# Kernel tuning notes

Hardware: AMD Instinct MI355X
Metric: run time of the kernel (lower is better)

## Reference

```python
import jax, jax.numpy as jnp
import numpy as np

DIM = 256
N_EMBED = 8192
DECAY = 0.1
COMMITMENT = 1.0
EPS = 1e-05


def setup_inputs() -> dict:
    key = jax.random.key(0)
    k1, k2, k3, k4 = jax.random.split(key, 4)
    return {
        "input": jax.random.normal(k1, (8, 1024, DIM), dtype=jnp.float32),
        "embed": jax.random.normal(k2, (DIM, N_EMBED), dtype=jnp.float32),
        "cluster_size": jax.random.uniform(k3, (N_EMBED,), dtype=jnp.float32),
        "embed_avg": jax.random.normal(k4, (DIM, N_EMBED), dtype=jnp.float32),
    }


def reference(input, embed, cluster_size, embed_avg):
    dtype = input.dtype
    flatten = input.reshape(-1, DIM)  # [N, dim]
    # squared euclidean distance to each code: [N, n_embed]
    dist = (
        jnp.sum(flatten * flatten, axis=1, keepdims=True)
        - 2.0 * (flatten @ embed)
        + jnp.sum(embed * embed, axis=0, keepdims=True)
    )
    embed_ind_flat = jnp.argmin(dist, axis=1)  # [N]
    embed_ind = embed_ind_flat.reshape(input.shape[:-1])
    quantize = jnp.take(embed.T, embed_ind, axis=0)  # [..., dim]

    # EMA codebook update (training path), via segment sums instead of dense one-hot
    bins = jax.ops.segment_sum(
        jnp.ones_like(embed_ind_flat, dtype=dtype), embed_ind_flat, num_segments=N_EMBED
    )  # one_hot.sum(0)
    embed_sum = jax.ops.segment_sum(flatten, embed_ind_flat, num_segments=N_EMBED).T  # [dim, n_embed]
    cluster_size_new = cluster_size * DECAY + (1.0 - DECAY) * bins
    embed_avg_new = embed_avg * DECAY + (1.0 - DECAY) * embed_sum
    smoothed = (cluster_size_new + EPS) / (jnp.sum(cluster_size_new) + N_EMBED * EPS)
    cs = smoothed * jnp.sum(cluster_size_new)
    embed_normalized = embed_avg_new / cs[None, :]

    commit_loss = jnp.mean((jax.lax.stop_gradient(quantize) - input) ** 2) * COMMITMENT
    quantize_st = input + jax.lax.stop_gradient(quantize - input)
    return (quantize_st, embed_ind, commit_loss, embed_normalized, cluster_size_new, embed_avg_new)
```

## Files before the change

### kernel.cpp

```cpp
#include <hip/hip_runtime.h>

typedef unsigned short u16;
typedef __attribute__((ext_vector_type(8))) short short8;
typedef __attribute__((ext_vector_type(4))) float f32x4;

#define DIM    256
#define NE     8192
#define NROWS  8192
#define DECAY  0.1f
#define EPS_F  1e-5f
#define CRANGES 16
#define CPH     8
#define MQ      384u

#define OUT_Q    0
#define OUT_IND  2097152
#define OUT_LOSS 2105344
#define OUT_NORM 2105345
#define OUT_CSN  4202497
#define OUT_AVG  4210689

#define WS_CAND  65536
#define WS_ENORM 1114112
#define WS_BASEQ 1146880
#define WS_SUM   1179648
#define WS_BINS  9568256
#define WS_LOSS  9601024
#define WS_SCS   9601032
#define WS_XB    9601040
#define WS_ETB   13795344
#define WS_ET32  17989648
#define WS_ZLEN  (WS_XB - WS_SUM)

__device__ __forceinline__ unsigned f32_ord(float f)
{
    unsigned u = __float_as_uint(f);
    return (u & 0x80000000u) ? ~u : (u | 0x80000000u);
}
__device__ __forceinline__ u16 bf16rne(float f)
{
    unsigned u = __float_as_uint(f);
    return (u16)((u + 0x7fffu + ((u >> 16) & 1u)) >> 16);
}
__device__ __forceinline__ void gload16(const void* g, void* l)
{
    __builtin_amdgcn_global_load_lds((const __attribute__((address_space(1))) unsigned int*)g,
                                     (__attribute__((address_space(3))) unsigned int*)l, 16, 0, 0);
}

__global__ __launch_bounds__(256) void vq_prep_k(const float* __restrict__ X,
                                                 const float* __restrict__ E,
                                                 const float* __restrict__ CS,
                                                 u16* __restrict__ Xb,
                                                 float* __restrict__ ET32,
                                                 u16* __restrict__ ETb,
                                                 float* __restrict__ enorm,
                                                 float* __restrict__ baseq,
                                                 double* __restrict__ sumcs)
{
    const int bid = blockIdx.x;
    const int t = threadIdx.x;

    if (bid < 128) {
        __shared__ float T[64][65];
        const int j0 = bid * 64;
        const int jc = t >> 2, seg = t & 3;
        const int j = j0 + jc;
        float esum = 0.f;
        for (int d0 = 0; d0 < DIM; d0 += 64) {
            if (d0) __syncthreads();
            #pragma unroll
            for (int p = 0; p < 4; ++p) {
                const int dr = p * 16 + (t >> 4);
                const float4 v = *(const float4*)(E + (size_t)(d0 + dr) * NE + j0 + (t & 15) * 4);
                T[dr][(t & 15) * 4 + 0] = v.x; T[dr][(t & 15) * 4 + 1] = v.y;
                T[dr][(t & 15) * 4 + 2] = v.z; T[dr][(t & 15) * 4 + 3] = v.w;
            }
            __syncthreads();
            float vals[16];
            #pragma unroll
            for (int i = 0; i < 16; ++i) vals[i] = T[seg * 16 + i][jc];
            float4* o32 = (float4*)(ET32 + (size_t)j * DIM + d0 + seg * 16);
            o32[0] = make_float4(vals[0], vals[1], vals[2], vals[3]);
            o32[1] = make_float4(vals[4], vals[5], vals[6], vals[7]);
            o32[2] = make_float4(vals[8], vals[9], vals[10], vals[11]);
            o32[3] = make_float4(vals[12], vals[13], vals[14], vals[15]);
            short8 b0, b1;
            #pragma unroll
            for (int i = 0; i < 8; ++i) { b0[i] = (short)bf16rne(vals[i]); b1[i] = (short)bf16rne(vals[8 + i]); }
            *(short8*)(ETb + (size_t)j * DIM + d0 + seg * 16) = b0;
            *(short8*)(ETb + (size_t)j * DIM + d0 + seg * 16 + 8) = b1;
            #pragma unroll
            for (int i = 0; i < 16; ++i) esum += vals[i] * vals[i];
        }
        esum += __shfl_xor(esum, 1, 4);
        esum += __shfl_xor(esum, 2, 4);
        if (seg == 0) {
            enorm[j] = esum;
            baseq[j] = (esum + 512.f) * 256.f;
        }
    } else if (bid < 256) {
        const int chunk = bid - 128;
        #pragma unroll
        for (int it = 0; it < 8; ++it) {
            const int gi = chunk * 2048 + it * 256 + t;
            const float4 a = ((const float4*)X)[gi * 2];
            const float4 b = ((const float4*)X)[gi * 2 + 1];
            short8 v;
            v[0] = (short)bf16rne(a.x); v[1] = (short)bf16rne(a.y);
            v[2] = (short)bf16rne(a.z); v[3] = (short)bf16rne(a.w);
            v[4] = (short)bf16rne(b.x); v[5] = (short)bf16rne(b.y);
            v[6] = (short)bf16rne(b.z); v[7] = (short)bf16rne(b.w);
            *(short8*)(Xb + (size_t)gi * 8) = v;
        }
    } else {
        double s = 0.0;
        #pragma unroll
        for (int it = 0; it < 8; ++it) {
            const float4 v = ((const float4*)CS)[it * 256 + t];
            s += (double)v.x + (double)v.y + (double)v.z + (double)v.w;
        }
        #pragma unroll
        for (int off = 32; off > 0; off >>= 1) s += __shfl_down(s, off);
        __shared__ double wred[4];
        if ((t & 63) == 0) wred[t >> 6] = s;
        __syncthreads();
        if (t == 0) sumcs[0] = wred[0] + wred[1] + wred[2] + wred[3];
    }
}

__global__ __launch_bounds__(256, 2) void vq_scan_k(const u16* __restrict__ Xb,
                                                    const u16* __restrict__ ETb,
                                                    const float* __restrict__ baseq,
                                                    unsigned* __restrict__ cand)
{
    __shared__ u16 Bs[2][32][512];

    const int tid = threadIdx.x;
    const int w = tid >> 6, l = tid & 63;
    const int lane16 = l & 15, g = l >> 4;
    const int rowbase = blockIdx.x * 256 + w * 64;
    const int c0 = blockIdx.y * 512;

    short8 af[4][8];
    #pragma unroll
    for (int sub = 0; sub < 4; ++sub)
        #pragma unroll
        for (int k8 = 0; k8 < 8; ++k8) {
            af[sub][k8] = *(const short8*)(Xb + (size_t)(rowbase + sub * 16 + lane16) * DIM + k8 * 32 + g * 8);
            asm volatile("" : "+a"(af[sub][k8]));
        }

    unsigned s0[16], s1[16];
    #pragma unroll
    for (int i = 0; i < 16; ++i) { s0[i] = 0xFFFFFFFFu; s1[i] = 0xFFFFFFFFu; }

    const u16* gsrc = ETb + (size_t)(c0 + lane16) * DIM + (size_t)w * 64 + g * 8;

    #pragma unroll
    for (int tt = 0; tt < 4; ++tt) {
        gload16(gsrc + (size_t)tt * 16 * DIM,      &Bs[0][tt * 8 + 2 * w + 0][0]);
        gload16(gsrc + (size_t)tt * 16 * DIM + 32, &Bs[0][tt * 8 + 2 * w + 1][0]);
    }
    asm volatile("s_waitcnt vmcnt(0)" ::: "memory");
    __builtin_amdgcn_s_barrier();

    int buf = 0;
    #pragma unroll 1
    for (int p = 0; p < CPH; ++p) {
        if (p + 1 < CPH) {
            const u16* nsrc = gsrc + (size_t)(p + 1) * 64 * DIM;
            #pragma unroll
            for (int tt = 0; tt < 4; ++tt) {
                gload16(nsrc + (size_t)tt * 16 * DIM,      &Bs[buf ^ 1][tt * 8 + 2 * w + 0][0]);
                gload16(nsrc + (size_t)tt * 16 * DIM + 32, &Bs[buf ^ 1][tt * 8 + 2 * w + 1][0]);
            }
        }
        #pragma unroll
        for (int half = 0; half < 4; ++half) {
            const int col = c0 + (p * 4 + half) * 16 + lane16;
            const float bq = baseq[col];
            f32x4 acc[4];
            #pragma unroll
            for (int sub = 0; sub < 4; ++sub) acc[sub] = {0.f, 0.f, 0.f, 0.f};
            __builtin_amdgcn_s_setprio(1);
            #pragma unroll
            for (int k8 = 0; k8 < 8; ++k8) {
                const short8 bf = *(const short8*)&Bs[buf][half * 8 + k8][l * 8];
                #pragma unroll
                for (int sub = 0; sub < 4; ++sub)
                    acc[sub] = __builtin_amdgcn_mfma_f32_16x16x32_bf16(af[sub][k8], bf, acc[sub], 0, 0, 0);
            }
            __builtin_amdgcn_s_setprio(0);
            #pragma unroll
            for (int sub = 0; sub < 4; ++sub)
                #pragma unroll
                for (int r = 0; r < 4; ++r) {
                    const int i = sub * 4 + r;
                    const float qf = fmaf(acc[sub][r], -512.f, bq);
                    const unsigned key = (((unsigned)qf) << 13) | (unsigned)col;
                    const unsigned tt = max(s0[i], key);
                    s0[i] = min(s0[i], key);
                    s1[i] = min(s1[i], tt);
                }
        }
        asm volatile("s_waitcnt vmcnt(0)" ::: "memory");
        __builtin_amdgcn_s_barrier();
        buf ^= 1;
    }

    #pragma unroll
    for (int m = 1; m < 16; m <<= 1) {
        #pragma unroll
        for (int i = 0; i < 16; ++i) {
            const unsigned o0 = __shfl_xor(s0[i], m);
            const unsigned o1 = __shfl_xor(s1[i], m);
            const unsigned t0 = min(s0[i], o0);
            const unsigned t1 = min(max(s0[i], o0), min(s1[i], o1));
            s0[i] = t0; s1[i] = t1;
        }
    }
    if (lane16 == 0) {
        #pragma unroll
        for (int i = 0; i < 16; ++i) {
            const int row = rowbase + (i >> 2) * 16 + g * 4 + (i & 3);
            cand[((size_t)row * CRANGES + blockIdx.y) * 2 + 0] = s0[i];
            cand[((size_t)row * CRANGES + blockIdx.y) * 2 + 1] = s1[i];
        }
    }
}

__global__ __launch_bounds__(256) void vq_finalize_k(const unsigned* __restrict__ cand,
                                                     const float* __restrict__ X,
                                                     const float* __restrict__ ET32,
                                                     const float* __restrict__ enorm,
                                                     float* __restrict__ out_q,
                                                     float* __restrict__ out_ind,
                                                     float* __restrict__ ws_sum,
                                                     float* __restrict__ bins,
                                                     double* __restrict__ loss)
{
    __shared__ int sj[4];
    const int tid = threadIdx.x;
    const int w = tid >> 6, l = tid & 63;
    const int row = blockIdx.x * 4 + w;

    unsigned key = 0xFFFFFFFFu;
    if (l < 32) key = cand[(size_t)row * 32 + l];
    unsigned qmin = key;
    #pragma unroll
    for (int m = 32; m; m >>= 1) qmin = min(qmin, __shfl_xor(qmin, m));
    const unsigned qthr = (qmin >> 13) + MQ;
    unsigned long long mask = __ballot((l < 32) && ((key >> 13) <= qthr));
    const float4 xv = *(const float4*)(X + (size_t)row * DIM + l * 4);
    unsigned long long best = 0xFFFFFFFFFFFFFFFFull;
    while (mask) {
        const int src = __builtin_ctzll(mask);
        mask &= mask - 1;
        const int col = (int)(__shfl(key, src) & 8191u);
        const float4 ev = *(const float4*)(ET32 + (size_t)col * DIM + l * 4);
        float s = xv.x * ev.x + xv.y * ev.y + xv.z * ev.z + xv.w * ev.w;
        #pragma unroll
        for (int m = 32; m; m >>= 1) s += __shfl_xor(s, m);
        const float d = enorm[col] - 2.f * s;
        const unsigned long long k64 = ((unsigned long long)f32_ord(d) << 32) | (unsigned)col;
        best = (k64 < best) ? k64 : best;
    }
    if (l == 0) {
        const int j = (int)(best & 8191u);
        sj[w] = j;
        out_ind[row] = (float)j;
    }
    __syncthreads();

    float lsum = 0.f;
    #pragma unroll
    for (int q = 0; q < 4; ++q) {
        const int r = blockIdx.x * 4 + q;
        const int j = sj[q];
        const float x  = X[(size_t)r * DIM + tid];
        const float qv = ET32[(size_t)j * DIM + tid];
        out_q[(size_t)r * DIM + tid] = x + (qv - x);
        const float d = qv - x;
        lsum += d * d;
        atomicAdd(&ws_sum[(size_t)j * DIM + tid], x);
        if (tid == 0) atomicAdd(&bins[j], 1.0f);
    }
    #pragma unroll
    for (int off = 32; off > 0; off >>= 1) lsum += __shfl_down(lsum, off);
    __shared__ double wred[4];
    if ((tid & 63) == 0) wred[tid >> 6] = (double)lsum;
    __syncthreads();
    if (tid == 0) atomicAdd(loss, wred[0] + wred[1] + wred[2] + wred[3]);
}

__global__ __launch_bounds__(256) void vq_embed_k(const float* __restrict__ EA,
                                                  const float* __restrict__ cs,
                                                  const float* __restrict__ bins,
                                                  const float* __restrict__ ws_sum,
                                                  const double* __restrict__ sumcs,
                                                  const double* __restrict__ loss,
                                                  float* __restrict__ out_norm,
                                                  float* __restrict__ out_avg,
                                                  float* __restrict__ out_csn,
                                                  float* __restrict__ out_loss)
{
    __shared__ float T[64][69];
    const int tid = threadIdx.x;
    const int j0 = blockIdx.x * 64;
    const int d0 = blockIdx.y * 64;
    #pragma unroll
    for (int p = 0; p < 4; ++p) {
        const int jr = (tid >> 4) + p * 16;
        const int dc = (tid & 15) * 4;
        const float4 v = *(const float4*)(ws_sum + (size_t)(j0 + jr) * DIM + d0 + dc);
        T[jr][dc + 0] = v.x; T[jr][dc + 1] = v.y; T[jr][dc + 2] = v.z; T[jr][dc + 3] = v.w;
    }
    __syncthreads();
    const double S = (double)DECAY * sumcs[0] + (double)(1.0f - DECAY) * (double)NROWS;
    const float fac = (float)(S / (S + (double)NE * 1e-5));
    const int jc = tid & 63;
    const int j  = j0 + jc;
    const float csn  = cs[j] * DECAY + (1.0f - DECAY) * bins[j];
    const float cs_j = (csn + EPS_F) * fac;
    if (blockIdx.y == 0 && tid < 64) out_csn[j0 + tid] = cs[j0 + tid] * DECAY + (1.0f - DECAY) * bins[j0 + tid];
    if (blockIdx.y == 0 && blockIdx.x == 0 && tid == 0) out_loss[0] = (float)(loss[0] * (1.0 / 2097152.0));
    const int drb = (tid >> 6) * 16;
    #pragma unroll
    for (int p = 0; p < 16; ++p) {
        const int dr = drb + p;
        const float sum = T[jc][dr];
        const float ea  = EA[(size_t)(d0 + dr) * NE + j];
        const float ean = DECAY * ea + (1.0f - DECAY) * sum;
        out_avg[(size_t)(d0 + dr) * NE + j]  = ean;
        out_norm[(size_t)(d0 + dr) * NE + j] = ean / cs_j;
    }
}

extern "C" void kernel_launch(void* const* d_in, const int* in_sizes, int n_in,
                              void* d_out, int out_size, void* d_ws, size_t ws_size,
                              hipStream_t stream)
{
    const float* X  = (const float*)d_in[0];
    const float* E  = (const float*)d_in[1];
    const float* CS = (const float*)d_in[2];
    const float* EA = (const float*)d_in[3];
    float* out = (float*)d_out;
    char*  ws  = (char*)d_ws;

    unsigned* cand  = (unsigned*)(ws + WS_CAND);
    float*  enorm  = (float*)(ws + WS_ENORM);
    float*  baseq  = (float*)(ws + WS_BASEQ);
    float*  ws_sum = (float*)(ws + WS_SUM);
    float*  bins   = (float*)(ws + WS_BINS);
    double* loss   = (double*)(ws + WS_LOSS);
    double* sumcs  = (double*)(ws + WS_SCS);
    u16*    Xb     = (u16*)(ws + WS_XB);
    u16*    ETb    = (u16*)(ws + WS_ETB);
    float*  ET32   = (float*)(ws + WS_ET32);

    hipMemsetAsync(ws + WS_SUM, 0, WS_ZLEN, stream);

    vq_prep_k<<<257, 256, 0, stream>>>(X, E, CS, Xb, ET32, ETb, enorm, baseq, sumcs);
    vq_scan_k<<<dim3(NROWS / 256, CRANGES), 256, 0, stream>>>(Xb, ETb, baseq, cand);
    vq_finalize_k<<<NROWS / 4, 256, 0, stream>>>(cand, X, ET32, enorm, out + OUT_Q, out + OUT_IND, ws_sum, bins, loss);
    vq_embed_k<<<dim3(NE / 64, DIM / 64), 256, 0, stream>>>(EA, CS, bins, ws_sum, sumcs, loss,
                                                            out + OUT_NORM, out + OUT_AVG, out + OUT_CSN, out + OUT_LOSS);
}
```

Baseline: 103.5 us.

## Halve scan tile rows per wave and codes per stage to raise occupancy

The distance-scan kernel now gives each wave 32 rows instead of 64 and stages 32 codes per double-buffer step instead of 64. This halves the A-fragment and top-2 register state and the LDS buffer, and launch bounds move from 2 to 4 blocks per SM with twice as many blocks launched. The prefetch wait becomes a partial vmcnt with the barrier at the top of each stage, and the MFMA priority boost is removed. In exchange, each B tile loaded from LDS feeds fewer MFMAs, so LDS traffic and global re-reads of the codebook per row double, and there are more barriers per unit of work.

Measured after the change: 106.6 us. +3.0%, slower.

```diff
diff --git a/kernel.cpp b/kernel.cpp
--- a/kernel.cpp
+++ b/kernel.cpp
@@ -10,7 +10,7 @@
 #define DECAY  0.1f
 #define EPS_F  1e-5f
 #define CRANGES 16
-#define CPH     8
+#define CPAIRS  16
 #define MQ      384u
 
 #define OUT_Q    0
@@ -129,71 +129,69 @@
     }
 }
 
-__global__ __launch_bounds__(256, 2) void vq_scan_k(const u16* __restrict__ Xb,
+__global__ __launch_bounds__(256, 4) void vq_scan_k(const u16* __restrict__ Xb,
                                                     const u16* __restrict__ ETb,
                                                     const float* __restrict__ baseq,
                                                     unsigned* __restrict__ cand)
 {
-    __shared__ u16 Bs[2][32][512];
+    __shared__ u16 Bs[2][16][512];
 
     const int tid = threadIdx.x;
     const int w = tid >> 6, l = tid & 63;
     const int lane16 = l & 15, g = l >> 4;
-    const int rowbase = blockIdx.x * 256 + w * 64;
+    const int rowbase = blockIdx.x * 128 + w * 32;
     const int c0 = blockIdx.y * 512;
 
-    short8 af[4][8];
-    #pragma unroll
-    for (int sub = 0; sub < 4; ++sub)
+    short8 af[2][8];
+    #pragma unroll
+    for (int sub = 0; sub < 2; ++sub)
         #pragma unroll
         for (int k8 = 0; k8 < 8; ++k8) {
             af[sub][k8] = *(const short8*)(Xb + (size_t)(rowbase + sub * 16 + lane16) * DIM + k8 * 32 + g * 8);
             asm volatile("" : "+a"(af[sub][k8]));
         }
 
-    unsigned s0[16], s1[16];
-    #pragma unroll
-    for (int i = 0; i < 16; ++i) { s0[i] = 0xFFFFFFFFu; s1[i] = 0xFFFFFFFFu; }
+    unsigned s0[8], s1[8];
+    #pragma unroll
+    for (int i = 0; i < 8; ++i) { s0[i] = 0xFFFFFFFFu; s1[i] = 0xFFFFFFFFu; }
 
     const u16* gsrc = ETb + (size_t)(c0 + lane16) * DIM + (size_t)w * 64 + g * 8;
 
-    #pragma unroll
-    for (int tt = 0; tt < 4; ++tt) {
-        gload16(gsrc + (size_t)tt * 16 * DIM,      &Bs[0][tt * 8 + 2 * w + 0][0]);
-        gload16(gsrc + (size_t)tt * 16 * DIM + 32, &Bs[0][tt * 8 + 2 * w + 1][0]);
-    }
-    asm volatile("s_waitcnt vmcnt(0)" ::: "memory");
-    __builtin_amdgcn_s_barrier();
+    gload16(gsrc,                 &Bs[0][2 * w + 0][0]);
+    gload16(gsrc + 32,            &Bs[0][2 * w + 1][0]);
+    gload16(gsrc + 16 * DIM,      &Bs[0][8 + 2 * w + 0][0]);
+    gload16(gsrc + 16 * DIM + 32, &Bs[0][8 + 2 * w + 1][0]);
 
     int buf = 0;
     #pragma unroll 1
-    for (int p = 0; p < CPH; ++p) {
-        if (p + 1 < CPH) {
-            const u16* nsrc = gsrc + (size_t)(p + 1) * 64 * DIM;
-            #pragma unroll
-            for (int tt = 0; tt < 4; ++tt) {
-                gload16(nsrc + (size_t)tt * 16 * DIM,      &Bs[buf ^ 1][tt * 8 + 2 * w + 0][0]);
-                gload16(nsrc + (size_t)tt * 16 * DIM + 32, &Bs[buf ^ 1][tt * 8 + 2 * w + 1][0]);
-            }
-        }
-        #pragma unroll
-        for (int half = 0; half < 4; ++half) {
-            const int col = c0 + (p * 4 + half) * 16 + lane16;
+    for (int p = 0; p < CPAIRS; ++p) {
+        if (p + 1 < CPAIRS) {
+            const u16* nsrc = gsrc + (size_t)(p + 1) * 32 * DIM;
+            gload16(nsrc,                 &Bs[buf ^ 1][2 * w + 0][0]);
+            gload16(nsrc + 32,            &Bs[buf ^ 1][2 * w + 1][0]);
+            gload16(nsrc + 16 * DIM,      &Bs[buf ^ 1][8 + 2 * w + 0][0]);
+            gload16(nsrc + 16 * DIM + 32, &Bs[buf ^ 1][8 + 2 * w + 1][0]);
+            asm volatile("s_waitcnt vmcnt(4)" ::: "memory");
+        } else {
+            asm volatile("s_waitcnt vmcnt(0)" ::: "memory");
+        }
+        __builtin_amdgcn_s_barrier();
+
+        #pragma unroll
+        for (int half = 0; half < 2; ++half) {
+            const int col = c0 + (p * 2 + half) * 16 + lane16;
             const float bq = baseq[col];
-            f32x4 acc[4];
-            #pragma unroll
-            for (int sub = 0; sub < 4; ++sub) acc[sub] = {0.f, 0.f, 0.f, 0.f};
-            __builtin_amdgcn_s_setprio(1);
+            f32x4 acc[2];
+            acc[0] = {0.f, 0.f, 0.f, 0.f};
+            acc[1] = {0.f, 0.f, 0.f, 0.f};
             #pragma unroll
             for (int k8 = 0; k8 < 8; ++k8) {
                 const short8 bf = *(const short8*)&Bs[buf][half * 8 + k8][l * 8];
-                #pragma unroll
-                for (int sub = 0; sub < 4; ++sub)
-                    acc[sub] = __builtin_amdgcn_mfma_f32_16x16x32_bf16(af[sub][k8], bf, acc[sub], 0, 0, 0);
+                acc[0] = __builtin_amdgcn_mfma_f32_16x16x32_bf16(af[0][k8], bf, acc[0], 0, 0, 0);
+                acc[1] = __builtin_amdgcn_mfma_f32_16x16x32_bf16(af[1][k8], bf, acc[1], 0, 0, 0);
             }
-            __builtin_amdgcn_s_setprio(0);
-            #pragma unroll
-            for (int sub = 0; sub < 4; ++sub)
+            #pragma unroll
+            for (int sub = 0; sub < 2; ++sub)
                 #pragma unroll
                 for (int r = 0; r < 4; ++r) {
                     const int i = sub * 4 + r;
@@ -204,7 +202,6 @@
                     s1[i] = min(s1[i], tt);
                 }
         }
-        asm volatile("s_waitcnt vmcnt(0)" ::: "memory");
         __builtin_amdgcn_s_barrier();
         buf ^= 1;
     }
@@ -212,7 +209,7 @@
     #pragma unroll
     for (int m = 1; m < 16; m <<= 1) {
         #pragma unroll
-        for (int i = 0; i < 16; ++i) {
+        for (int i = 0; i < 8; ++i) {
             const unsigned o0 = __shfl_xor(s0[i], m);
             const unsigned o1 = __shfl_xor(s1[i], m);
             const unsigned t0 = min(s0[i], o0);
@@ -222,7 +219,7 @@
     }
     if (lane16 == 0) {
         #pragma unroll
-        for (int i = 0; i < 16; ++i) {
+        for (int i = 0; i < 8; ++i) {
             const int row = rowbase + (i >> 2) * 16 + g * 4 + (i & 3);
             cand[((size_t)row * CRANGES + blockIdx.y) * 2 + 0] = s0[i];
             cand[((size_t)row * CRANGES + blockIdx.y) * 2 + 1] = s1[i];
@@ -362,7 +359,7 @@
     hipMemsetAsync(ws + WS_SUM, 0, WS_ZLEN, stream);
 
     vq_prep_k<<<257, 256, 0, stream>>>(X, E, CS, Xb, ET32, ETb, enorm, baseq, sumcs);
-    vq_scan_k<<<dim3(NROWS / 256, CRANGES), 256, 0, stream>>>(Xb, ETb, baseq, cand);
+    vq_scan_k<<<dim3(NROWS / 128, CRANGES), 256, 0, stream>>>(Xb, ETb, baseq, cand);
     vq_finalize_k<<<NROWS / 4, 256, 0, stream>>>(cand, X, ET32, enorm, out + OUT_Q, out + OUT_IND, ws_sum, bins, loss);
     vq_embed_k<<<dim3(NE / 64, DIM / 64), 256, 0, stream>>>(EA, CS, bins, ws_sum, sumcs, loss,
                                                             out + OUT_NORM, out + OUT_AVG, out + OUT_CSN, out + OUT_LOSS);
```

## Use 4-stage 16-column LDS ring pipeline with partial vmcnt waits in scan kernel

Applied to the files above, without the earlier changes.

Replaces the double-buffered 64-column LDS staging in the distance-scan kernel with a 4-slot ring of 16-column tiles, prefetched three tiles ahead. Partial vmcnt waits let loads for later tiles stay in flight while the current tile is computed. The per-column baseq values are now staged once into LDS instead of being read from global memory in the inner loop. LDS use drops, but there is one barrier per 16-column tile instead of per 64, so barrier count rises fourfold.

Result: slower. 110.6 us (+6.9%).

```diff
diff --git a/kernel.cpp b/kernel.cpp
--- a/kernel.cpp
+++ b/kernel.cpp
@@ -10,7 +10,7 @@
 #define DECAY  0.1f
 #define EPS_F  1e-5f
 #define CRANGES 16
-#define CPH     8
+#define CTILES  32
 #define MQ      384u
 
 #define OUT_Q    0
@@ -134,7 +134,8 @@
                                                     const float* __restrict__ baseq,
                                                     unsigned* __restrict__ cand)
 {
-    __shared__ u16 Bs[2][32][512];
+    __shared__ u16 Bs[4][8][512];
+    __shared__ float Bq[512];
 
     const int tid = threadIdx.x;
     const int w = tid >> 6, l = tid & 63;
@@ -151,6 +152,8 @@
             asm volatile("" : "+a"(af[sub][k8]));
         }
 
+    const float2 bq2 = *(const float2*)(baseq + c0 + tid * 2);
+
     unsigned s0[16], s1[16];
     #pragma unroll
     for (int i = 0; i < 16; ++i) { s0[i] = 0xFFFFFFFFu; s1[i] = 0xFFFFFFFFu; }
@@ -158,55 +161,54 @@
     const u16* gsrc = ETb + (size_t)(c0 + lane16) * DIM + (size_t)w * 64 + g * 8;
 
     #pragma unroll
-    for (int tt = 0; tt < 4; ++tt) {
-        gload16(gsrc + (size_t)tt * 16 * DIM,      &Bs[0][tt * 8 + 2 * w + 0][0]);
-        gload16(gsrc + (size_t)tt * 16 * DIM + 32, &Bs[0][tt * 8 + 2 * w + 1][0]);
+    for (int tt = 0; tt < 3; ++tt) {
+        gload16(gsrc + (size_t)tt * 16 * DIM,      &Bs[tt][2 * w + 0][0]);
+        gload16(gsrc + (size_t)tt * 16 * DIM + 32, &Bs[tt][2 * w + 1][0]);
     }
     asm volatile("s_waitcnt vmcnt(0)" ::: "memory");
-    __builtin_amdgcn_s_barrier();
-
-    int buf = 0;
+    *(float2*)&Bq[tid * 2] = bq2;
+    __syncthreads();
+
     #pragma unroll 1
-    for (int p = 0; p < CPH; ++p) {
-        if (p + 1 < CPH) {
-            const u16* nsrc = gsrc + (size_t)(p + 1) * 64 * DIM;
-            #pragma unroll
-            for (int tt = 0; tt < 4; ++tt) {
-                gload16(nsrc + (size_t)tt * 16 * DIM,      &Bs[buf ^ 1][tt * 8 + 2 * w + 0][0]);
-                gload16(nsrc + (size_t)tt * 16 * DIM + 32, &Bs[buf ^ 1][tt * 8 + 2 * w + 1][0]);
+    for (int ct = 0; ct < CTILES; ++ct) {
+        if (ct < 30)       asm volatile("s_waitcnt vmcnt(4)" ::: "memory");
+        else if (ct == 30) asm volatile("s_waitcnt vmcnt(2)" ::: "memory");
+        else               asm volatile("s_waitcnt vmcnt(0)" ::: "memory");
+        __builtin_amdgcn_s_barrier();
+
+        if (ct + 3 < CTILES) {
+            const u16* nsrc = gsrc + (size_t)(ct + 3) * 16 * DIM;
+            gload16(nsrc,      &Bs[(ct + 3) & 3][2 * w + 0][0]);
+            gload16(nsrc + 32, &Bs[(ct + 3) & 3][2 * w + 1][0]);
+        }
+
+        const int slot = ct & 3;
+        const float bq = Bq[ct * 16 + lane16];
+        f32x4 acc[4];
+        #pragma unroll
+        for (int sub = 0; sub < 4; ++sub) acc[sub] = {0.f, 0.f, 0.f, 0.f};
+        __builtin_amdgcn_s_setprio(1);
+        #pragma unroll
+        for (int k8 = 0; k8 < 8; ++k8) {
+            const short8 bf = *(const short8*)&Bs[slot][k8][l * 8];
+            #pragma unroll
+            for (int sub = 0; sub < 4; ++sub)
+                acc[sub] = __builtin_amdgcn_mfma_f32_16x16x32_bf16(af[sub][k8], bf, acc[sub], 0, 0, 0);
+        }
+        __builtin_amdgcn_s_setprio(0);
+
+        const int col = c0 + ct * 16 + lane16;
+        #pragma unroll
+        for (int sub = 0; sub < 4; ++sub)
+            #pragma unroll
+            for (int r = 0; r < 4; ++r) {
+                const int i = sub * 4 + r;
+                const float qf = fmaf(acc[sub][r], -512.f, bq);
+                const unsigned key = (((unsigned)qf) << 13) | (unsigned)col;
+                const unsigned tt = max(s0[i], key);
+                s0[i] = min(s0[i], key);
+                s1[i] = min(s1[i], tt);
             }
-        }
-        #pragma unroll
-        for (int half = 0; half < 4; ++half) {
-            const int col = c0 + (p * 4 + half) * 16 + lane16;
-            const float bq = baseq[col];
-            f32x4 acc[4];
-            #pragma unroll
-            for (int sub = 0; sub < 4; ++sub) acc[sub] = {0.f, 0.f, 0.f, 0.f};
-            __builtin_amdgcn_s_setprio(1);
-            #pragma unroll
-            for (int k8 = 0; k8 < 8; ++k8) {
-                const short8 bf = *(const short8*)&Bs[buf][half * 8 + k8][l * 8];
-                #pragma unroll
-                for (int sub = 0; sub < 4; ++sub)
-                    acc[sub] = __builtin_amdgcn_mfma_f32_16x16x32_bf16(af[sub][k8], bf, acc[sub], 0, 0, 0);
-            }
-            __builtin_amdgcn_s_setprio(0);
-            #pragma unroll
-            for (int sub = 0; sub < 4; ++sub)
-                #pragma unroll
-                for (int r = 0; r < 4; ++r) {
-                    const int i = sub * 4 + r;
-                    const float qf = fmaf(acc[sub][r], -512.f, bq);
-                    const unsigned key = (((unsigned)qf) << 13) | (unsigned)col;
-                    const unsigned tt = max(s0[i], key);
-                    s0[i] = min(s0[i], key);
-                    s1[i] = min(s1[i], tt);
-                }
-        }
-        asm volatile("s_waitcnt vmcnt(0)" ::: "memory");
-        __builtin_amdgcn_s_barrier();
-        buf ^= 1;
     }
 
     #pragma unroll
```
